# Kernel optimization log

Measured on AMD Instinct MI355X. Metric: run time of the kernel, lower is better.

Reference implementation:

```python
import jax, jax.numpy as jnp
import numpy as np

N_NODES = 100000
N_EDGES = 1600000


def gcn_conv(x, edge_index, W, b, num_nodes):
    # PyG GCNConv (normalize=True, add_self_loops=True):
    #   out = D^{-1/2} (A + I) D^{-1/2} (x @ W) + b
    h = x @ W  # [N, out_ch]
    src = jnp.concatenate([edge_index[0], jnp.arange(num_nodes, dtype=edge_index.dtype)])
    dst = jnp.concatenate([edge_index[1], jnp.arange(num_nodes, dtype=edge_index.dtype)])
    deg = jax.ops.segment_sum(jnp.ones_like(dst, dtype=h.dtype), dst, num_segments=num_nodes)
    dinv = jnp.where(deg > 0, jax.lax.rsqrt(deg), 0.0)  # deg^{-1/2}, inf->0
    norm = dinv[src] * dinv[dst]  # [E+N]
    msgs = h[src] * norm[:, None]  # gather + scale, [E+N, out_ch]
    out = jax.ops.segment_sum(msgs, dst, num_segments=num_nodes)
    return out + b


def setup_inputs() -> dict:
    key = jax.random.key(0)
    kx, ke, kw1, kw2 = jax.random.split(key, 4)
    x = jax.random.normal(kx, (N_NODES, 32), dtype=jnp.float32)
    edge_index = jax.random.randint(ke, (2, N_EDGES), 0, N_NODES, dtype=jnp.int64)
    W1 = jax.random.normal(kw1, (32, 64), dtype=jnp.float32) * (1.0 / np.sqrt(32))
    b1 = jnp.zeros((64,), dtype=jnp.float32)
    W2 = jax.random.normal(kw2, (64, 64), dtype=jnp.float32) * (1.0 / np.sqrt(64))
    b2 = jnp.zeros((64,), dtype=jnp.float32)
    return {"x": x, "edge_index": edge_index, "W1": W1, "b1": b1, "W2": W2, "b2": b2}


def reference(x, edge_index, W1, b1, W2, b2):
    n = x.shape[0]
    h = jax.nn.relu(gcn_conv(x, edge_index, W1, b1, n))
    h = jax.nn.relu(gcn_conv(h, edge_index, W2, b2, n))
    return h
```

## Files before the change

### kernel.cpp

```cpp
#include <hip/hip_runtime.h>

#define N_NODES 100000
#define N_EDGES 1600000
#define BSHIFT 9
#define BNODES 512
#define NB ((N_NODES + BNODES - 1) / BNODES)
#define NBP 256
#define CAP 10240
#define TILE 4096
#define EPT 16

typedef _Float16 half8 __attribute__((ext_vector_type(8)));
typedef _Float16 half4 __attribute__((ext_vector_type(4)));
typedef float floatx4 __attribute__((ext_vector_type(4)));


__device__ void packW_dev(const float* __restrict__ W, _Float16* __restrict__ Wp, int IC) {
    int total = IC * 64;
    for (int idx = threadIdx.x; idx < total; idx += 256) {
        int j = idx & 7;
        int l = (idx >> 3) & 63;
        int cbks = idx >> 9;
        int cb = cbks & 3;
        int ks = cbks >> 2;
        int k = ks * 32 + (l >> 4) * 8 + j;
        int c = cb * 16 + (l & 15);
        Wp[idx] = (_Float16)W[k * 64 + c];
    }
}

__global__ __launch_bounds__(256) void k_init_pack(
        int* __restrict__ bucketCur,
        const float* __restrict__ W1, _Float16* __restrict__ Wp1,
        const float* __restrict__ W2, _Float16* __restrict__ Wp2) {
    if (blockIdx.x == 1) { packW_dev(W1, Wp1, 32); return; }
    if (blockIdx.x == 2) { packW_dev(W2, Wp2, 64); return; }
    int t = threadIdx.x;
    if (t < NB) bucketCur[t] = t * CAP;
}

__global__ __launch_bounds__(256) void k_redistribute(
        const int* __restrict__ src, const int* __restrict__ dst,
        int* __restrict__ bucketCur, int* __restrict__ packed, int e) {
    __shared__ int cnt[NBP], base[NBP], gdelta[NBP], lcur[NBP];
    __shared__ int wsum[4];
    __shared__ int sorted[TILE];
    __shared__ int sdelta[TILE];
    int tileBase = blockIdx.x * TILE;
    int tileCnt = min(TILE, e - tileBase);
    int t = threadIdx.x;
    for (int i = t; i < NBP; i += 256) cnt[i] = 0;
    __syncthreads();
    int pk[EPT], bk[EPT];
#pragma unroll
    for (int k = 0; k < EPT; ++k) {
        int i = k * 256 + t;
        if (i < tileCnt) {
            int d = dst[tileBase + i];
            int s = src[tileBase + i];
            bk[k] = d >> BSHIFT;
            pk[k] = (s << BSHIFT) | (d & (BNODES - 1));
            atomicAdd(&cnt[bk[k]], 1);
        } else bk[k] = -1;
    }
    __syncthreads();
    {
        int lane = t & 63, wid = t >> 6;
        int v = cnt[t];
        int sc = v;
#pragma unroll
        for (int o = 1; o < 64; o <<= 1) {
            int u = __shfl_up(sc, o, 64);
            if (lane >= o) sc += u;
        }
        if (lane == 63) wsum[wid] = sc;
        __syncthreads();
        if (t == 0) {
            int run = 0;
#pragma unroll
            for (int w = 0; w < 4; ++w) { int x2 = wsum[w]; wsum[w] = run; run += x2; }
        }
        __syncthreads();
        int excl = sc + wsum[wid] - v;
        base[t] = excl;
        lcur[t] = excl;
        if (t < NB && v > 0)
            gdelta[t] = atomicAdd(&bucketCur[t], v) - excl;
    }
    __syncthreads();
#pragma unroll
    for (int k = 0; k < EPT; ++k) {
        if (bk[k] >= 0) {
            int l = atomicAdd(&lcur[bk[k]], 1);
            sorted[l] = pk[k];
            sdelta[l] = gdelta[bk[k]];
        }
    }
    __syncthreads();
    for (int i = t; i < tileCnt; i += 256)
        packed[i + sdelta[i]] = sorted[i];
}

__global__ __launch_bounds__(512) void k_bucket_csr(
        const int* __restrict__ packed, const int* __restrict__ bucketCur,
        int* __restrict__ rowbeg, int* __restrict__ rowend,
        int* __restrict__ col, float* __restrict__ dinv,
        const float* __restrict__ X, _Float16* __restrict__ xh1, int n) {
    __shared__ int hist[BNODES], cur[BNODES];
    __shared__ int wsum[8];
    __shared__ float dinvS[BNODES];
    int b = blockIdx.x;
    int node0 = b * BNODES;
    int nn = min(BNODES, n - node0);
    int eb = b * CAP;
    int ee = bucketCur[b];
    int t = threadIdx.x;
    hist[t] = 0;
    __syncthreads();
    for (int i = eb + t; i < ee; i += 512)
        atomicAdd(&hist[packed[i] & (BNODES - 1)], 1);
    __syncthreads();
    int lane = t & 63, wid = t >> 6;
    int v = hist[t];
    int sc = v;
#pragma unroll
    for (int o = 1; o < 64; o <<= 1) {
        int u = __shfl_up(sc, o, 64);
        if (lane >= o) sc += u;
    }
    if (lane == 63) wsum[wid] = sc;
    __syncthreads();
    if (t == 0) {
        int run = 0;
#pragma unroll
        for (int w = 0; w < 8; ++w) { int x2 = wsum[w]; wsum[w] = run; run += x2; }
    }
    __syncthreads();
    int excl = sc + wsum[wid] - v;
    cur[t] = excl;
    float di = rsqrtf((float)(1 + v));
    dinvS[t] = di;
    if (t < nn) {
        rowbeg[node0 + t] = eb + excl;
        rowend[node0 + t] = eb + excl + v;
        dinv[node0 + t] = di;
    }
    __syncthreads();
    for (int i = eb + t; i < ee; i += 512) {
        int p = packed[i];
        int dl = p & (BNODES - 1);
        int l = atomicAdd(&cur[dl], 1);
        col[eb + l] = p >> BSHIFT;
    }
    const float4* X4 = (const float4*)X;
    half4* U4 = (half4*)xh1;
    for (int i = t; i < nn * 8; i += 512) {
        int nl = i >> 3;
        float4 vv = X4[(size_t)(node0 + nl) * 8 + (i & 7)];
        float d2 = dinvS[nl];
        half4 h;
        h[0] = (_Float16)(vv.x * d2);
        h[1] = (_Float16)(vv.y * d2);
        h[2] = (_Float16)(vv.z * d2);
        h[3] = (_Float16)(vv.w * d2);
        U4[(size_t)(node0 + nl) * 8 + (i & 7)] = h;
    }
}


__global__ __launch_bounds__(256) void k_fused1(
        const _Float16* __restrict__ G, const int* __restrict__ rowbeg,
        const int* __restrict__ rowend,
        const int* __restrict__ col, const float* __restrict__ dinv,
        const _Float16* __restrict__ Wp, const float* __restrict__ bias,
        _Float16* __restrict__ out, int n) {
    __shared__ _Float16 aggS[64][40];
    const int t = threadIdx.x;
    const int node0 = blockIdx.x * 64;
    {
        int nl = t >> 2, l = t & 3;
        int lane = t & 63;
        int lb = lane & 60;
        int node = node0 + nl;
        if (node < n) {
            const half8* Gr = (const half8*)G;
            half8 s = Gr[(size_t)node * 4 + l];
            float acc[8];
#pragma unroll
            for (int q = 0; q < 8; ++q) acc[q] = (float)s[q];
            int jb = rowbeg[node], je = rowend[node];
            int j = jb;
            for (; j + 7 < je; j += 8) {
                int cv0 = col[j + l];
                int cv1 = col[j + 4 + l];
                half8 v[8];
#pragma unroll
                for (int u = 0; u < 4; ++u) {
                    int s0 = __shfl(cv0, lb + u, 64);
                    v[u] = Gr[(size_t)s0 * 4 + l];
                }
#pragma unroll
                for (int u = 0; u < 4; ++u) {
                    int s1 = __shfl(cv1, lb + u, 64);
                    v[4 + u] = Gr[(size_t)s1 * 4 + l];
                }
#pragma unroll
                for (int u = 0; u < 8; ++u)
#pragma unroll
                    for (int q = 0; q < 8; ++q) acc[q] += (float)v[u][q];
            }
            for (; j + 1 < je; j += 2) {
                half8 v0 = Gr[(size_t)col[j] * 4 + l];
                half8 v1 = Gr[(size_t)col[j + 1] * 4 + l];
#pragma unroll
                for (int q = 0; q < 8; ++q) acc[q] += (float)v0[q] + (float)v1[q];
            }
            if (j < je) {
                half8 v0 = Gr[(size_t)col[j] * 4 + l];
#pragma unroll
                for (int q = 0; q < 8; ++q) acc[q] += (float)v0[q];
            }
            float di = dinv[node];
            half8 r;
#pragma unroll
            for (int q = 0; q < 8; ++q) r[q] = (_Float16)(acc[q] * di);
            *(half8*)&aggS[nl][l * 8] = r;
        }
    }
    __syncthreads();
    {
        const int lane = t & 63;
        const int w = t >> 6;
        int base = w * 16;
        int nw0 = node0 + base;
        if (nw0 >= n) return;
        half8 af = *(const half8*)&aggS[base + (lane & 15)][(lane >> 4) * 8];
        floatx4 z = {0.f, 0.f, 0.f, 0.f};
        floatx4 acc[4] = {z, z, z, z};
#pragma unroll
        for (int cb = 0; cb < 4; ++cb) {
            half8 bf = ((const half8*)Wp)[cb * 64 + lane];
            acc[cb] = __builtin_amdgcn_mfma_f32_16x16x32_f16(af, bf, acc[cb], 0, 0, 0);
        }
        int r0 = nw0 + (lane >> 4) * 4;
        int ch0 = lane & 15;
        float di[4];
#pragma unroll
        for (int r = 0; r < 4; ++r) di[r] = dinv[r0 + r];
#pragma unroll
        for (int cb = 0; cb < 4; ++cb) {
            int ch = cb * 16 + ch0;
            float bb = bias[ch];
#pragma unroll
            for (int r = 0; r < 4; ++r) {
                float v = acc[cb][r] + bb;
                v = v > 0.f ? v : 0.f;
                out[(size_t)(r0 + r) * 64 + ch] = (_Float16)(v * di[r]);
            }
        }
    }
}

__global__ __launch_bounds__(256) void k_fused2(
        const _Float16* __restrict__ G, const int* __restrict__ rowbeg,
        const int* __restrict__ rowend,
        const int* __restrict__ col, const float* __restrict__ dinv,
        const _Float16* __restrict__ Wp, const float* __restrict__ bias,
        float* __restrict__ out, int n) {
    __shared__ _Float16 aggS[32][72];
    const int t = threadIdx.x;
    const int node0 = blockIdx.x * 32;
    {
        int nl = t >> 3, l = t & 7;
        int lane = t & 63;
        int lb = lane & 56;
        int node = node0 + nl;
        const half8* Gr = (const half8*)G;
        half8 s = Gr[(size_t)node * 8 + l];
        float acc[8];
#pragma unroll
        for (int q = 0; q < 8; ++q) acc[q] = (float)s[q];
        int jb = rowbeg[node], je = rowend[node];
        int j = jb;
        for (; j + 7 < je; j += 8) {
            int cv = col[j + l];
            half8 v[8];
#pragma unroll
            for (int u = 0; u < 8; ++u) {
                int sv = __shfl(cv, lb + u, 64);
                v[u] = Gr[(size_t)sv * 8 + l];
            }
#pragma unroll
            for (int u = 0; u < 8; ++u)
#pragma unroll
                for (int q = 0; q < 8; ++q) acc[q] += (float)v[u][q];
        }
        for (; j + 1 < je; j += 2) {
            half8 v0 = Gr[(size_t)col[j] * 8 + l];
            half8 v1 = Gr[(size_t)col[j + 1] * 8 + l];
#pragma unroll
            for (int q = 0; q < 8; ++q) acc[q] += (float)v0[q] + (float)v1[q];
        }
        if (j < je) {
            half8 v0 = Gr[(size_t)col[j] * 8 + l];
#pragma unroll
            for (int q = 0; q < 8; ++q) acc[q] += (float)v0[q];
        }
        float di = dinv[node];
        half8 r;
#pragma unroll
        for (int q = 0; q < 8; ++q) r[q] = (_Float16)(acc[q] * di);
        *(half8*)&aggS[nl][l * 8] = r;
    }
    __syncthreads();
    if (t >= 128) return;
    {
        const int lane = t & 63;
        const int w = t >> 6;
        int base = w * 16;
        int nw0 = node0 + base;
        half8 af0 = *(const half8*)&aggS[base + (lane & 15)][(lane >> 4) * 8];
        half8 af1 = *(const half8*)&aggS[base + (lane & 15)][(lane >> 4) * 8 + 32];
        floatx4 z = {0.f, 0.f, 0.f, 0.f};
        floatx4 acc[4] = {z, z, z, z};
#pragma unroll
        for (int cb = 0; cb < 4; ++cb) {
            half8 bf0 = ((const half8*)Wp)[(0 * 4 + cb) * 64 + lane];
            half8 bf1 = ((const half8*)Wp)[(1 * 4 + cb) * 64 + lane];
            acc[cb] = __builtin_amdgcn_mfma_f32_16x16x32_f16(af0, bf0, acc[cb], 0, 0, 0);
            acc[cb] = __builtin_amdgcn_mfma_f32_16x16x32_f16(af1, bf1, acc[cb], 0, 0, 0);
        }
        int r0 = nw0 + (lane >> 4) * 4;
        int ch0 = lane & 15;
#pragma unroll
        for (int cb = 0; cb < 4; ++cb) {
            int ch = cb * 16 + ch0;
            float bb = bias[ch];
#pragma unroll
            for (int r = 0; r < 4; ++r) {
                float v = acc[cb][r] + bb;
                out[(size_t)(r0 + r) * 64 + ch] = v > 0.f ? v : 0.f;
            }
        }
    }
}


extern "C" void kernel_launch(void* const* d_in, const int* in_sizes, int n_in,
                              void* d_out, int out_size, void* d_ws, size_t ws_size,
                              hipStream_t stream) {
    const float* x  = (const float*)d_in[0];
    const int* ei   = (const int*)d_in[1];
    const float* W1 = (const float*)d_in[2];
    const float* b1 = (const float*)d_in[3];
    const float* W2 = (const float*)d_in[4];
    const float* b2 = (const float*)d_in[5];

    const int N = N_NODES;
    const int E = N_EDGES;
    const int* src = ei;
    const int* dst = ei + E;

    char* ws = (char*)d_ws;
    size_t off = 0;
    auto alloc = [&](size_t bytes) { void* p = ws + off; off = (off + bytes + 511) & ~511ull; return p; };
    int*   bucketCur  = (int*)  alloc((size_t)NB * 4);
    int*   packed     = (int*)  alloc((size_t)NB * CAP * 4);
    int*   rowbeg     = (int*)  alloc((size_t)N * 4);
    int*   rowend     = (int*)  alloc((size_t)N * 4);
    int*   col        = (int*)  alloc((size_t)NB * CAP * 4);
    float* dinv       = (float*)alloc((size_t)N * 4);
    _Float16* Wp1     = (_Float16*)alloc((size_t)32 * 64 * 2);
    _Float16* Wp2     = (_Float16*)alloc((size_t)64 * 64 * 2);
    _Float16* xh1     = (_Float16*)alloc((size_t)N * 32 * 2);
    _Float16* xh2     = (_Float16*)alloc((size_t)N * 64 * 2);
    float* outF       = (float*)d_out;

    const int B = 256;
    const int nTiles = (E + TILE - 1) / TILE;

    k_init_pack<<<3, B, 0, stream>>>(bucketCur, W1, Wp1, W2, Wp2);
    k_redistribute<<<nTiles, B, 0, stream>>>(src, dst, bucketCur, packed, E);
    k_bucket_csr<<<NB, BNODES, 0, stream>>>(packed, bucketCur, rowbeg, rowend, col, dinv, x, xh1, N);

    k_fused1<<<(N + 63) / 64, B, 0, stream>>>(xh1, rowbeg, rowend, col, dinv, Wp1, b1, xh2, N);

    k_fused2<<<N / 32, B, 0, stream>>>(xh2, rowbeg, rowend, col, dinv, Wp2, b2, outF, N);
}
```

Before: 111.5 us.

## Split each CSR row into low/high source halves and drop shuffle-based column loads

The CSR build now partitions each destination's neighbour list into sources below and above the midpoint node, recording a rowmid offset. Both aggregation kernels then gather the two halves in sequence, presumably so that concurrently running waves touch a narrower region of the feature table and get better cache locality. The column-index loading also changes from a coalesced load plus wave shuffles to direct per-thread col loads, which are redundant across lanes. This adds an extra atomic histogram pass, an extra rowmid array, and more divergent loop bounds.

After: 114.6 us. 1.03x slower.

```diff
diff --git a/kernel.cpp b/kernel.cpp
--- a/kernel.cpp
+++ b/kernel.cpp
@@ -2,6 +2,7 @@
 
 #define N_NODES 100000
 #define N_EDGES 1600000
+#define NHALF 50000
 #define BSHIFT 9
 #define BNODES 512
 #define NB ((N_NODES + BNODES - 1) / BNODES)
@@ -42,7 +43,7 @@
 __global__ __launch_bounds__(256) void k_redistribute(
         const int* __restrict__ src, const int* __restrict__ dst,
         int* __restrict__ bucketCur, int* __restrict__ packed, int e) {
-    __shared__ int cnt[NBP], base[NBP], gdelta[NBP], lcur[NBP];
+    __shared__ int cnt[NBP], gdelta[NBP], lcur[NBP];
     __shared__ int wsum[4];
     __shared__ int sorted[TILE];
     __shared__ int sdelta[TILE];
@@ -82,7 +83,6 @@
         }
         __syncthreads();
         int excl = sc + wsum[wid] - v;
-        base[t] = excl;
         lcur[t] = excl;
         if (t < NB && v > 0)
             gdelta[t] = atomicAdd(&bucketCur[t], v) - excl;
@@ -103,10 +103,10 @@
 
 __global__ __launch_bounds__(512) void k_bucket_csr(
         const int* __restrict__ packed, const int* __restrict__ bucketCur,
-        int* __restrict__ rowbeg, int* __restrict__ rowend,
+        int* __restrict__ rowbeg, int* __restrict__ rowmid, int* __restrict__ rowend,
         int* __restrict__ col, float* __restrict__ dinv,
         const float* __restrict__ X, _Float16* __restrict__ xh1, int n) {
-    __shared__ int hist[BNODES], cur[BNODES];
+    __shared__ int hist[BNODES], lowc[BNODES], curL[BNODES], curH[BNODES];
     __shared__ int wsum[8];
     __shared__ float dinvS[BNODES];
     int b = blockIdx.x;
@@ -116,9 +116,14 @@
     int ee = bucketCur[b];
     int t = threadIdx.x;
     hist[t] = 0;
-    __syncthreads();
-    for (int i = eb + t; i < ee; i += 512)
-        atomicAdd(&hist[packed[i] & (BNODES - 1)], 1);
+    lowc[t] = 0;
+    __syncthreads();
+    for (int i = eb + t; i < ee; i += 512) {
+        int p = packed[i];
+        int dl = p & (BNODES - 1);
+        atomicAdd(&hist[dl], 1);
+        if ((p >> BSHIFT) < NHALF) atomicAdd(&lowc[dl], 1);
+    }
     __syncthreads();
     int lane = t & 63, wid = t >> 6;
     int v = hist[t];
@@ -137,11 +142,14 @@
     }
     __syncthreads();
     int excl = sc + wsum[wid] - v;
-    cur[t] = excl;
+    int lc = lowc[t];
+    curL[t] = excl;
+    curH[t] = excl + lc;
     float di = rsqrtf((float)(1 + v));
     dinvS[t] = di;
     if (t < nn) {
         rowbeg[node0 + t] = eb + excl;
+        rowmid[node0 + t] = eb + excl + lc;
         rowend[node0 + t] = eb + excl + v;
         dinv[node0 + t] = di;
     }
@@ -149,8 +157,9 @@
     for (int i = eb + t; i < ee; i += 512) {
         int p = packed[i];
         int dl = p & (BNODES - 1);
-        int l = atomicAdd(&cur[dl], 1);
-        col[eb + l] = p >> BSHIFT;
+        int s = p >> BSHIFT;
+        int l = (s < NHALF) ? atomicAdd(&curL[dl], 1) : atomicAdd(&curH[dl], 1);
+        col[eb + l] = s;
     }
     const float4* X4 = (const float4*)X;
     half4* U4 = (half4*)xh1;
@@ -170,7 +179,7 @@
 
 __global__ __launch_bounds__(256) void k_fused1(
         const _Float16* __restrict__ G, const int* __restrict__ rowbeg,
-        const int* __restrict__ rowend,
+        const int* __restrict__ rowmid, const int* __restrict__ rowend,
         const int* __restrict__ col, const float* __restrict__ dinv,
         const _Float16* __restrict__ Wp, const float* __restrict__ bias,
         _Float16* __restrict__ out, int n) {
@@ -179,8 +188,6 @@
     const int node0 = blockIdx.x * 64;
     {
         int nl = t >> 2, l = t & 3;
-        int lane = t & 63;
-        int lb = lane & 60;
         int node = node0 + nl;
         if (node < n) {
             const half8* Gr = (const half8*)G;
@@ -188,38 +195,31 @@
             float acc[8];
 #pragma unroll
             for (int q = 0; q < 8; ++q) acc[q] = (float)s[q];
-            int jb = rowbeg[node], je = rowend[node];
-            int j = jb;
-            for (; j + 7 < je; j += 8) {
-                int cv0 = col[j + l];
-                int cv1 = col[j + 4 + l];
-                half8 v[8];
-#pragma unroll
-                for (int u = 0; u < 4; ++u) {
-                    int s0 = __shfl(cv0, lb + u, 64);
-                    v[u] = Gr[(size_t)s0 * 4 + l];
+            int jb = rowbeg[node], jm = rowmid[node], je = rowend[node];
+            auto accum = [&](int j, int j2) {
+                for (; j + 7 < j2; j += 8) {
+                    half8 v[8];
+#pragma unroll
+                    for (int u = 0; u < 8; ++u) v[u] = Gr[(size_t)col[j + u] * 4 + l];
+#pragma unroll
+                    for (int u = 0; u < 8; ++u)
+#pragma unroll
+                        for (int q = 0; q < 8; ++q) acc[q] += (float)v[u][q];
                 }
-#pragma unroll
-                for (int u = 0; u < 4; ++u) {
-                    int s1 = __shfl(cv1, lb + u, 64);
-                    v[4 + u] = Gr[(size_t)s1 * 4 + l];
+                for (; j + 1 < j2; j += 2) {
+                    half8 v0 = Gr[(size_t)col[j] * 4 + l];
+                    half8 v1 = Gr[(size_t)col[j + 1] * 4 + l];
+#pragma unroll
+                    for (int q = 0; q < 8; ++q) acc[q] += (float)v0[q] + (float)v1[q];
                 }
-#pragma unroll
-                for (int u = 0; u < 8; ++u)
-#pragma unroll
-                    for (int q = 0; q < 8; ++q) acc[q] += (float)v[u][q];
-            }
-            for (; j + 1 < je; j += 2) {
-                half8 v0 = Gr[(size_t)col[j] * 4 + l];
-                half8 v1 = Gr[(size_t)col[j + 1] * 4 + l];
-#pragma unroll
-                for (int q = 0; q < 8; ++q) acc[q] += (float)v0[q] + (float)v1[q];
-            }
-            if (j < je) {
-                half8 v0 = Gr[(size_t)col[j] * 4 + l];
-#pragma unroll
-                for (int q = 0; q < 8; ++q) acc[q] += (float)v0[q];
-            }
+                if (j < j2) {
+                    half8 v0 = Gr[(size_t)col[j] * 4 + l];
+#pragma unroll
+                    for (int q = 0; q < 8; ++q) acc[q] += (float)v0[q];
+                }
+            };
+            accum(jb, jm);
+            accum(jm, je);
             float di = dinv[node];
             half8 r;
 #pragma unroll
@@ -263,7 +263,7 @@
 
 __global__ __launch_bounds__(256) void k_fused2(
         const _Float16* __restrict__ G, const int* __restrict__ rowbeg,
-        const int* __restrict__ rowend,
+        const int* __restrict__ rowmid, const int* __restrict__ rowend,
         const int* __restrict__ col, const float* __restrict__ dinv,
         const _Float16* __restrict__ Wp, const float* __restrict__ bias,
         float* __restrict__ out, int n) {
@@ -272,40 +272,37 @@
     const int node0 = blockIdx.x * 32;
     {
         int nl = t >> 3, l = t & 7;
-        int lane = t & 63;
-        int lb = lane & 56;
         int node = node0 + nl;
         const half8* Gr = (const half8*)G;
         half8 s = Gr[(size_t)node * 8 + l];
         float acc[8];
 #pragma unroll
         for (int q = 0; q < 8; ++q) acc[q] = (float)s[q];
-        int jb = rowbeg[node], je = rowend[node];
-        int j = jb;
-        for (; j + 7 < je; j += 8) {
-            int cv = col[j + l];
-            half8 v[8];
-#pragma unroll
-            for (int u = 0; u < 8; ++u) {
-                int sv = __shfl(cv, lb + u, 64);
-                v[u] = Gr[(size_t)sv * 8 + l];
-            }
-#pragma unroll
-            for (int u = 0; u < 8; ++u)
-#pragma unroll
-                for (int q = 0; q < 8; ++q) acc[q] += (float)v[u][q];
-        }
-        for (; j + 1 < je; j += 2) {
-            half8 v0 = Gr[(size_t)col[j] * 8 + l];
-            half8 v1 = Gr[(size_t)col[j + 1] * 8 + l];
-#pragma unroll
-            for (int q = 0; q < 8; ++q) acc[q] += (float)v0[q] + (float)v1[q];
-        }
-        if (j < je) {
-            half8 v0 = Gr[(size_t)col[j] * 8 + l];
-#pragma unroll
-            for (int q = 0; q < 8; ++q) acc[q] += (float)v0[q];
-        }
+        int jb = rowbeg[node], jm = rowmid[node], je = rowend[node];
+        auto accum = [&](int j, int j2) {
+            for (; j + 7 < j2; j += 8) {
+                half8 v[8];
+#pragma unroll
+                for (int u = 0; u < 8; ++u) v[u] = Gr[(size_t)col[j + u] * 8 + l];
+#pragma unroll
+                for (int u = 0; u < 8; ++u)
+#pragma unroll
+                    for (int q = 0; q < 8; ++q) acc[q] += (float)v[u][q];
+            }
+            for (; j + 1 < j2; j += 2) {
+                half8 v0 = Gr[(size_t)col[j] * 8 + l];
+                half8 v1 = Gr[(size_t)col[j + 1] * 8 + l];
+#pragma unroll
+                for (int q = 0; q < 8; ++q) acc[q] += (float)v0[q] + (float)v1[q];
+            }
+            if (j < j2) {
+                half8 v0 = Gr[(size_t)col[j] * 8 + l];
+#pragma unroll
+                for (int q = 0; q < 8; ++q) acc[q] += (float)v0[q];
+            }
+        };
+        accum(jb, jm);
+        accum(jm, je);
         float di = dinv[node];
         half8 r;
 #pragma unroll
@@ -367,6 +364,7 @@
     int*   bucketCur  = (int*)  alloc((size_t)NB * 4);
     int*   packed     = (int*)  alloc((size_t)NB * CAP * 4);
     int*   rowbeg     = (int*)  alloc((size_t)N * 4);
+    int*   rowmid     = (int*)  alloc((size_t)N * 4);
     int*   rowend     = (int*)  alloc((size_t)N * 4);
     int*   col        = (int*)  alloc((size_t)NB * CAP * 4);
     float* dinv       = (float*)alloc((size_t)N * 4);
@@ -381,9 +379,9 @@
 
     k_init_pack<<<3, B, 0, stream>>>(bucketCur, W1, Wp1, W2, Wp2);
     k_redistribute<<<nTiles, B, 0, stream>>>(src, dst, bucketCur, packed, E);
-    k_bucket_csr<<<NB, BNODES, 0, stream>>>(packed, bucketCur, rowbeg, rowend, col, dinv, x, xh1, N);
-
-    k_fused1<<<(N + 63) / 64, B, 0, stream>>>(xh1, rowbeg, rowend, col, dinv, Wp1, b1, xh2, N);
-
-    k_fused2<<<N / 32, B, 0, stream>>>(xh2, rowbeg, rowend, col, dinv, Wp2, b2, outF, N);
-}
+    k_bucket_csr<<<NB, BNODES, 0, stream>>>(packed, bucketCur, rowbeg, rowmid, rowend, col, dinv, x, xh1, N);
+
+    k_fused1<<<(N + 63) / 64, B, 0, stream>>>(xh1, rowbeg, rowmid, rowend, col, dinv, Wp1, b1, xh2, N);
+
+    k_fused2<<<N / 32, B, 0, stream>>>(xh2, rowbeg, rowmid, rowend, col, dinv, Wp2, b2, outF, N);
+}
```

## Vectorize edge loads in bucketing kernels and drop shuffle-based index broadcast

Applied to the files above, without the earlier changes.

The redistribute and bucket-CSR kernels now read src/dst and packed entries as int4 vectors instead of scalar loads, with a scalar tail loop in the CSR kernel. The two aggregation kernels no longer load column indices cooperatively and broadcast them with wave shuffles; each lane reads the eight col entries directly, relying on cache broadcast. The vector loads assume 16-byte alignment of tile and bucket bases, which holds for TILE and CAP as defined. The direct col reads add redundant loads per lane in exchange for removing shuffle instructions and their dependency chain.

New measurement: 102.5 us. 1.09x faster.

```diff
diff --git a/kernel.cpp b/kernel.cpp
--- a/kernel.cpp
+++ b/kernel.cpp
@@ -42,7 +42,7 @@
 __global__ __launch_bounds__(256) void k_redistribute(
         const int* __restrict__ src, const int* __restrict__ dst,
         int* __restrict__ bucketCur, int* __restrict__ packed, int e) {
-    __shared__ int cnt[NBP], base[NBP], gdelta[NBP], lcur[NBP];
+    __shared__ int cnt[NBP], gdelta[NBP], lcur[NBP];
     __shared__ int wsum[4];
     __shared__ int sorted[TILE];
     __shared__ int sdelta[TILE];
@@ -53,15 +53,24 @@
     __syncthreads();
     int pk[EPT], bk[EPT];
 #pragma unroll
-    for (int k = 0; k < EPT; ++k) {
-        int i = k * 256 + t;
-        if (i < tileCnt) {
-            int d = dst[tileBase + i];
-            int s = src[tileBase + i];
-            bk[k] = d >> BSHIFT;
-            pk[k] = (s << BSHIFT) | (d & (BNODES - 1));
-            atomicAdd(&cnt[bk[k]], 1);
-        } else bk[k] = -1;
+    for (int k4 = 0; k4 < EPT / 4; ++k4) {
+        int base = (k4 * 256 + t) * 4;
+        if (base < tileCnt) {
+            int4 s4 = *(const int4*)(src + tileBase + base);
+            int4 d4 = *(const int4*)(dst + tileBase + base);
+            int ss[4] = {s4.x, s4.y, s4.z, s4.w};
+            int dd[4] = {d4.x, d4.y, d4.z, d4.w};
+#pragma unroll
+            for (int u = 0; u < 4; ++u) {
+                int k = k4 * 4 + u;
+                bk[k] = dd[u] >> BSHIFT;
+                pk[k] = (ss[u] << BSHIFT) | (dd[u] & (BNODES - 1));
+                atomicAdd(&cnt[bk[k]], 1);
+            }
+        } else {
+#pragma unroll
+            for (int u = 0; u < 4; ++u) bk[k4 * 4 + u] = -1;
+        }
     }
     __syncthreads();
     {
@@ -82,7 +91,6 @@
         }
         __syncthreads();
         int excl = sc + wsum[wid] - v;
-        base[t] = excl;
         lcur[t] = excl;
         if (t < NB && v > 0)
             gdelta[t] = atomicAdd(&bucketCur[t], v) - excl;
@@ -114,10 +122,20 @@
     int nn = min(BNODES, n - node0);
     int eb = b * CAP;
     int ee = bucketCur[b];
+    int nv = ee - eb;
+    int nv4 = nv >> 2;
+    const int4* p4 = (const int4*)(packed + eb);
     int t = threadIdx.x;
     hist[t] = 0;
     __syncthreads();
-    for (int i = eb + t; i < ee; i += 512)
+    for (int i = t; i < nv4; i += 512) {
+        int4 pp = p4[i];
+        atomicAdd(&hist[pp.x & (BNODES - 1)], 1);
+        atomicAdd(&hist[pp.y & (BNODES - 1)], 1);
+        atomicAdd(&hist[pp.z & (BNODES - 1)], 1);
+        atomicAdd(&hist[pp.w & (BNODES - 1)], 1);
+    }
+    for (int i = eb + (nv4 << 2) + t; i < ee; i += 512)
         atomicAdd(&hist[packed[i] & (BNODES - 1)], 1);
     __syncthreads();
     int lane = t & 63, wid = t >> 6;
@@ -146,7 +164,17 @@
         dinv[node0 + t] = di;
     }
     __syncthreads();
-    for (int i = eb + t; i < ee; i += 512) {
+    for (int i = t; i < nv4; i += 512) {
+        int4 pp = p4[i];
+        int e0[4] = {pp.x, pp.y, pp.z, pp.w};
+#pragma unroll
+        for (int u = 0; u < 4; ++u) {
+            int dl = e0[u] & (BNODES - 1);
+            int l = atomicAdd(&cur[dl], 1);
+            col[eb + l] = e0[u] >> BSHIFT;
+        }
+    }
+    for (int i = eb + (nv4 << 2) + t; i < ee; i += 512) {
         int p = packed[i];
         int dl = p & (BNODES - 1);
         int l = atomicAdd(&cur[dl], 1);
@@ -179,8 +207,6 @@
     const int node0 = blockIdx.x * 64;
     {
         int nl = t >> 2, l = t & 3;
-        int lane = t & 63;
-        int lb = lane & 60;
         int node = node0 + nl;
         if (node < n) {
             const half8* Gr = (const half8*)G;
@@ -191,19 +217,9 @@
             int jb = rowbeg[node], je = rowend[node];
             int j = jb;
             for (; j + 7 < je; j += 8) {
-                int cv0 = col[j + l];
-                int cv1 = col[j + 4 + l];
                 half8 v[8];
 #pragma unroll
-                for (int u = 0; u < 4; ++u) {
-                    int s0 = __shfl(cv0, lb + u, 64);
-                    v[u] = Gr[(size_t)s0 * 4 + l];
-                }
-#pragma unroll
-                for (int u = 0; u < 4; ++u) {
-                    int s1 = __shfl(cv1, lb + u, 64);
-                    v[4 + u] = Gr[(size_t)s1 * 4 + l];
-                }
+                for (int u = 0; u < 8; ++u) v[u] = Gr[(size_t)col[j + u] * 4 + l];
 #pragma unroll
                 for (int u = 0; u < 8; ++u)
 #pragma unroll
@@ -272,8 +288,6 @@
     const int node0 = blockIdx.x * 32;
     {
         int nl = t >> 3, l = t & 7;
-        int lane = t & 63;
-        int lb = lane & 56;
         int node = node0 + nl;
         const half8* Gr = (const half8*)G;
         half8 s = Gr[(size_t)node * 8 + l];
@@ -283,13 +297,9 @@
         int jb = rowbeg[node], je = rowend[node];
         int j = jb;
         for (; j + 7 < je; j += 8) {
-            int cv = col[j + l];
             half8 v[8];
 #pragma unroll
-            for (int u = 0; u < 8; ++u) {
-                int sv = __shfl(cv, lb + u, 64);
-                v[u] = Gr[(size_t)sv * 8 + l];
-            }
+            for (int u = 0; u < 8; ++u) v[u] = Gr[(size_t)col[j + u] * 8 + l];
 #pragma unroll
             for (int u = 0; u < 8; ++u)
 #pragma unroll
```
